# Optimization experiments

Hardware: AMD Instinct MI355X
Metric: run time of the kernel (lower is better)

Reference implementation:

```python
import jax, jax.numpy as jnp
import numpy as np

D_MODEL, D_STATE, N_HEADS = 1024, 64, 16


def setup_inputs() -> dict:
    key = jax.random.key(0)
    ks = jax.random.split(key, 4)
    B, T = 4, 4096
    s = 1.0 / np.sqrt(D_MODEL)
    x = jax.random.normal(ks[0], (B, T, D_MODEL), dtype=jnp.float32)
    h_prev = jnp.zeros((B, N_HEADS, D_STATE), dtype=jnp.float32)
    gate_w = jax.random.normal(ks[1], (2 * N_HEADS * D_STATE, D_MODEL), dtype=jnp.float32) * s
    # torch init: forget-gate bias = 1, input-gate bias = 0
    gate_b = jnp.concatenate([jnp.ones(N_HEADS * D_STATE), jnp.zeros(N_HEADS * D_STATE)]).astype(jnp.float32)
    value_w = jax.random.normal(ks[2], (N_HEADS * D_STATE, D_MODEL), dtype=jnp.float32) * s
    out_w = jax.random.normal(ks[3], (D_MODEL, N_HEADS * D_STATE), dtype=jnp.float32) * s
    return {"x": x, "h_prev": h_prev, "gate_w": gate_w, "gate_b": gate_b, "value_w": value_w, "out_w": out_w}


def reference(x, h_prev, gate_w, gate_b, value_w, out_w):
    B, T, _ = x.shape
    H, S = N_HEADS, D_STATE
    gates = (jnp.einsum('btd,gd->btg', x, gate_w) + gate_b).reshape(B, T, 2, H, S)
    A = jax.nn.sigmoid(gates[:, :, 0])   # [B,T,H,S] forget gate
    Bg = jax.nn.sigmoid(gates[:, :, 1])  # [B,T,H,S] input gate
    V = jnp.einsum('btd,vd->btv', x, value_w).reshape(B, T, H, S)

    def step(h, inp):
        a_t, bv_t = inp
        h = a_t * h + bv_t
        return h, h

    # time-major for scan; precompute B*V elementwise product
    a_tm = jnp.moveaxis(A, 1, 0)                # [T,B,H,S]
    bv_tm = jnp.moveaxis(Bg * V, 1, 0)          # [T,B,H,S]
    h_last, h_seq = jax.lax.scan(step, h_prev, (a_tm, bv_tm))
    h_flat = jnp.moveaxis(h_seq, 0, 1).reshape(B, T, H * S)
    y = jnp.einsum('btv,dv->btd', h_flat, out_w)  # dropout is identity at p=0/eval
    return y, h_last
```

## Files before the change

### kernel.cpp

```cpp
#include <hip/hip_runtime.h>
#include <cstdint>
#include <cstddef>


typedef __bf16 bf16;
typedef __bf16 bf16x8 __attribute__((ext_vector_type(8)));
typedef float  f32x4  __attribute__((ext_vector_type(4)));

__device__ __forceinline__ void gload_lds16(const void* g, void* l) {
  __builtin_amdgcn_global_load_lds(
      (const __attribute__((address_space(1))) void*)g,
      (__attribute__((address_space(3))) void*)l, 16, 0, 0);
}

__device__ __forceinline__ float sigmoidf_(float x) {
  return 1.0f / (1.0f + __expf(-x));
}

__global__ __launch_bounds__(256) void cast_f32_to_bf16(
    const float* __restrict__ src, bf16* __restrict__ dst, int n8) {
  int i = blockIdx.x * 256 + threadIdx.x;
  if (i >= n8) return;
  const float4* s4 = (const float4*)src;
  float4 v0 = s4[2 * i], v1 = s4[2 * i + 1];
  bf16x8 o;
  o[0] = (bf16)v0.x; o[1] = (bf16)v0.y; o[2] = (bf16)v0.z; o[3] = (bf16)v0.w;
  o[4] = (bf16)v1.x; o[5] = (bf16)v1.y; o[6] = (bf16)v1.z; o[7] = (bf16)v1.w;
  *(bf16x8*)(dst + (size_t)i * 8) = o;
}

template <int MCOLS, int EPI>
__global__ __launch_bounds__(256, 3) void gemm_bt(
    const bf16* __restrict__ A, const bf16* __restrict__ Bw,
    const float* __restrict__ gate_b,
    float* __restrict__ o0, float* __restrict__ o1, float* __restrict__ o2) {
  constexpr int K = 1024;
  __shared__ __align__(16) bf16 As[128 * 64];
  __shared__ __align__(16) bf16 Bs[128 * 64];
  const int tid  = threadIdx.x;
  const int lane = tid & 63;
  const int quad = lane >> 4;
  const int wv   = tid >> 6;
  const int wrow = wv & 1, wcol = wv >> 1;
  const int n0 = blockIdx.y * 128;
  const int m0 = blockIdx.x * 128;

  const bf16* ga[4];
  const bf16* gb[4];
  bf16* la[4];
  bf16* lb[4];
#pragma unroll
  for (int j = 0; j < 4; ++j) {
    int s   = j * 256 + tid;
    int row = s >> 3;
    int kc  = (s & 7) ^ (row & 7);
    ga[j] = A  + (size_t)(n0 + row) * K + kc * 8;
    gb[j] = Bw + (size_t)(m0 + row) * K + kc * 8;
    la[j] = &As[s * 8];
    lb[j] = &Bs[s * 8];
  }

  f32x4 acc[4][4];
#pragma unroll
  for (int mi = 0; mi < 4; ++mi)
#pragma unroll
    for (int ni = 0; ni < 4; ++ni) acc[mi][ni] = (f32x4){0.f, 0.f, 0.f, 0.f};

  for (int k0 = 0; k0 < K; k0 += 64) {
#pragma unroll
    for (int j = 0; j < 4; ++j) gload_lds16(ga[j], la[j]);
#pragma unroll
    for (int j = 0; j < 4; ++j) gload_lds16(gb[j], lb[j]);
#pragma unroll
    for (int j = 0; j < 4; ++j) { ga[j] += 64; gb[j] += 64; }
    __syncthreads();
#pragma unroll
    for (int kk = 0; kk < 2; ++kk) {
      bf16x8 af[4], bfv[4];
#pragma unroll
      for (int mi = 0; mi < 4; ++mi) {
        int row  = wrow * 64 + mi * 16 + (lane & 15);
        int slot = row * 8 + ((kk * 4 + quad) ^ (row & 7));
        af[mi] = *(const bf16x8*)(&As[slot * 8]);
      }
#pragma unroll
      for (int ni = 0; ni < 4; ++ni) {
        int row  = wcol * 64 + ni * 16 + (lane & 15);
        int slot = row * 8 + ((kk * 4 + quad) ^ (row & 7));
        bfv[ni] = *(const bf16x8*)(&Bs[slot * 8]);
      }
#pragma unroll
      for (int mi = 0; mi < 4; ++mi)
#pragma unroll
        for (int ni = 0; ni < 4; ++ni)
          acc[mi][ni] = __builtin_amdgcn_mfma_f32_16x16x32_bf16(
              af[mi], bfv[ni], acc[mi][ni], 0, 0, 0);
    }
    __syncthreads();
  }

#pragma unroll
  for (int mi = 0; mi < 4; ++mi) {
#pragma unroll
    for (int ni = 0; ni < 4; ++ni) {
      const int m = m0 + wcol * 64 + ni * 16 + (lane & 15);
#pragma unroll
      for (int r = 0; r < 4; ++r) {
        const int n = n0 + wrow * 64 + mi * 16 + quad * 4 + r;
        float val = acc[mi][ni][r];
        if (EPI == 0) {
          if (m < 2048) {
            float sv = sigmoidf_(val + gate_b[m]);
            if (m < 1024)
              o0[(size_t)n * 1024 + m] = sv;
            else
              o1[(size_t)n * 1024 + (m - 1024)] = sv;
          } else {
            o2[(size_t)n * 1024 + (m - 2048)] = val;
          }
        } else {
          o0[(size_t)n * MCOLS + m] = val;
        }
      }
    }
  }
}

__global__ __launch_bounds__(256) void scan_pass1(
    const float* __restrict__ a, const float* __restrict__ bg,
    const float* __restrict__ v, float* __restrict__ Ac,
    float* __restrict__ Uc) {
  const int c = blockIdx.x * 256 + threadIdx.x;
  const int j = blockIdx.y;
  const int b = blockIdx.z;
  const size_t base = ((size_t)(b * 4096 + j * 128)) * 1024 + c;
  const float* pa = a + base;
  const float* pg = bg + base;
  const float* pv = v + base;
  float P = 1.f, U = 0.f;
#pragma unroll 4
  for (int t = 0; t < 128; ++t) {
    float at  = pa[(size_t)t * 1024];
    float bvt = pg[(size_t)t * 1024] * pv[(size_t)t * 1024];
    P *= at;
    U = at * U + bvt;
  }
  const size_t o = ((size_t)(b * 32 + j)) * 1024 + c;
  Ac[o] = P;
  Uc[o] = U;
}

__global__ __launch_bounds__(256) void scan_pass2(
    const float* __restrict__ Ac, const float* __restrict__ Uc,
    const float* __restrict__ h_prev, float* __restrict__ Hs,
    float* __restrict__ hlast) {
  const int id = blockIdx.x * 256 + threadIdx.x;
  const int b = id >> 10, c = id & 1023;
  float H = h_prev[b * 1024 + c];
  for (int j = 0; j < 32; ++j) {
    const size_t o = ((size_t)(b * 32 + j)) * 1024 + c;
    Hs[o] = H;
    H = Ac[o] * H + Uc[o];
  }
  hlast[b * 1024 + c] = H;
}

__global__ __launch_bounds__(256) void scan_pass3(
    const float* __restrict__ a, const float* __restrict__ bg,
    const float* __restrict__ v, const float* __restrict__ Hs,
    bf16* __restrict__ hb) {
  const int c = blockIdx.x * 256 + threadIdx.x;
  const int j = blockIdx.y;
  const int b = blockIdx.z;
  const size_t base = ((size_t)(b * 4096 + j * 128)) * 1024 + c;
  const float* pa = a + base;
  const float* pg = bg + base;
  const float* pv = v + base;
  bf16* ph = hb + base;
  float h = Hs[((size_t)(b * 32 + j)) * 1024 + c];
#pragma unroll 4
  for (int t = 0; t < 128; ++t) {
    float at  = pa[(size_t)t * 1024];
    float bvt = pg[(size_t)t * 1024] * pv[(size_t)t * 1024];
    h = at * h + bvt;
    ph[(size_t)t * 1024] = (bf16)h;
  }
}

extern "C" void kernel_launch(void* const* d_in, const int* in_sizes, int n_in,
                              void* d_out, int out_size, void* d_ws,
                              size_t ws_size, hipStream_t stream) {
  const float* x       = (const float*)d_in[0];
  const float* h_prev  = (const float*)d_in[1];
  const float* gate_w  = (const float*)d_in[2];
  const float* gate_b  = (const float*)d_in[3];
  const float* value_w = (const float*)d_in[4];
  const float* out_w   = (const float*)d_in[5];
  float* out = (float*)d_out;

  char* ws = (char*)d_ws;
  bf16*  xb   = (bf16*)(ws);
  bf16*  wgv  = (bf16*)(ws + 33554432);
  bf16*  owb  = (bf16*)(ws + 39845888);
  float* g1   = (float*)(ws + 41943040);
  float* vbuf = (float*)(ws + 109051904);
  float* Ac   = (float*)(ws + 176160768);
  float* Uc   = (float*)(ws + 176685056);
  float* Hs   = (float*)(ws + 177209344);
  bf16*  hb   = xb;
  float* abuf = out;
  float* hlast = out + 16777216;

  cast_f32_to_bf16<<<8192, 256, 0, stream>>>(x, xb, 2097152);
  cast_f32_to_bf16<<<1024, 256, 0, stream>>>(gate_w, wgv, 262144);
  cast_f32_to_bf16<<<512, 256, 0, stream>>>(value_w, wgv + 2048 * 1024, 131072);
  cast_f32_to_bf16<<<512, 256, 0, stream>>>(out_w, owb, 131072);

  gemm_bt<3072, 0><<<dim3(24, 128), 256, 0, stream>>>(xb, wgv, gate_b, abuf,
                                                      g1, vbuf);

  scan_pass1<<<dim3(4, 32, 4), 256, 0, stream>>>(abuf, g1, vbuf, Ac, Uc);
  scan_pass2<<<16, 256, 0, stream>>>(Ac, Uc, h_prev, Hs, hlast);
  scan_pass3<<<dim3(4, 32, 4), 256, 0, stream>>>(abuf, g1, vbuf, Hs, hb);

  gemm_bt<1024, 1><<<dim3(8, 128), 256, 0, stream>>>(hb, owb, nullptr, out,
                                                     nullptr, nullptr);
}
```

Measured before the change: 406.2 us.

## Store gate and value intermediates in fp16 and switch GEMMs to f16 MFMA

Switches the GEMM operands from bf16 to fp16 and writes the sigmoid gates and value projections as fp16 instead of fp32, halving intermediate traffic between the gate GEMM and the scan passes. The scan passes now read f16x2 pairs, with each thread handling two channels, and accumulate in fp32. This trades reduced memory bandwidth for lower-precision storage of the gates and values, and fp16 range limits could affect accuracy.

```diff
diff --git a/kernel.cpp b/kernel.cpp
--- a/kernel.cpp
+++ b/kernel.cpp
@@ -3,9 +3,10 @@
 #include <cstddef>
 
 
-typedef __bf16 bf16;
-typedef __bf16 bf16x8 __attribute__((ext_vector_type(8)));
-typedef float  f32x4  __attribute__((ext_vector_type(4)));
+typedef _Float16 f16;
+typedef _Float16 f16x2 __attribute__((ext_vector_type(2)));
+typedef _Float16 f16x8 __attribute__((ext_vector_type(8)));
+typedef float    f32x4 __attribute__((ext_vector_type(4)));
 
 __device__ __forceinline__ void gload_lds16(const void* g, void* l) {
   __builtin_amdgcn_global_load_lds(
@@ -17,26 +18,26 @@
   return 1.0f / (1.0f + __expf(-x));
 }
 
-__global__ __launch_bounds__(256) void cast_f32_to_bf16(
-    const float* __restrict__ src, bf16* __restrict__ dst, int n8) {
+__global__ __launch_bounds__(256) void cast_f32_to_f16(
+    const float* __restrict__ src, f16* __restrict__ dst, int n8) {
   int i = blockIdx.x * 256 + threadIdx.x;
   if (i >= n8) return;
   const float4* s4 = (const float4*)src;
   float4 v0 = s4[2 * i], v1 = s4[2 * i + 1];
-  bf16x8 o;
-  o[0] = (bf16)v0.x; o[1] = (bf16)v0.y; o[2] = (bf16)v0.z; o[3] = (bf16)v0.w;
-  o[4] = (bf16)v1.x; o[5] = (bf16)v1.y; o[6] = (bf16)v1.z; o[7] = (bf16)v1.w;
-  *(bf16x8*)(dst + (size_t)i * 8) = o;
-}
-
-template <int MCOLS, int EPI>
+  f16x8 o;
+  o[0] = (f16)v0.x; o[1] = (f16)v0.y; o[2] = (f16)v0.z; o[3] = (f16)v0.w;
+  o[4] = (f16)v1.x; o[5] = (f16)v1.y; o[6] = (f16)v1.z; o[7] = (f16)v1.w;
+  *(f16x8*)(dst + (size_t)i * 8) = o;
+}
+
+template <int EPI>
 __global__ __launch_bounds__(256, 3) void gemm_bt(
-    const bf16* __restrict__ A, const bf16* __restrict__ Bw,
+    const f16* __restrict__ A, const f16* __restrict__ Bw,
     const float* __restrict__ gate_b,
-    float* __restrict__ o0, float* __restrict__ o1, float* __restrict__ o2) {
+    void* __restrict__ o0v, void* __restrict__ o1v, void* __restrict__ o2v) {
   constexpr int K = 1024;
-  __shared__ __align__(16) bf16 As[128 * 64];
-  __shared__ __align__(16) bf16 Bs[128 * 64];
+  __shared__ __align__(16) f16 As[128 * 64];
+  __shared__ __align__(16) f16 Bs[128 * 64];
   const int tid  = threadIdx.x;
   const int lane = tid & 63;
   const int quad = lane >> 4;
@@ -45,10 +46,10 @@
   const int n0 = blockIdx.y * 128;
   const int m0 = blockIdx.x * 128;
 
-  const bf16* ga[4];
-  const bf16* gb[4];
-  bf16* la[4];
-  bf16* lb[4];
+  const f16* ga[4];
+  const f16* gb[4];
+  f16* la[4];
+  f16* lb[4];
 #pragma unroll
   for (int j = 0; j < 4; ++j) {
     int s   = j * 256 + tid;
@@ -76,24 +77,24 @@
     __syncthreads();
 #pragma unroll
     for (int kk = 0; kk < 2; ++kk) {
-      bf16x8 af[4], bfv[4];
+      f16x8 af[4], bfv[4];
 #pragma unroll
       for (int mi = 0; mi < 4; ++mi) {
         int row  = wrow * 64 + mi * 16 + (lane & 15);
         int slot = row * 8 + ((kk * 4 + quad) ^ (row & 7));
-        af[mi] = *(const bf16x8*)(&As[slot * 8]);
+        af[mi] = *(const f16x8*)(&As[slot * 8]);
       }
 #pragma unroll
       for (int ni = 0; ni < 4; ++ni) {
         int row  = wcol * 64 + ni * 16 + (lane & 15);
         int slot = row * 8 + ((kk * 4 + quad) ^ (row & 7));
-        bfv[ni] = *(const bf16x8*)(&Bs[slot * 8]);
+        bfv[ni] = *(const f16x8*)(&Bs[slot * 8]);
       }
 #pragma unroll
       for (int mi = 0; mi < 4; ++mi)
 #pragma unroll
         for (int ni = 0; ni < 4; ++ni)
-          acc[mi][ni] = __builtin_amdgcn_mfma_f32_16x16x32_bf16(
+          acc[mi][ni] = __builtin_amdgcn_mfma_f32_16x16x32_f16(
               af[mi], bfv[ni], acc[mi][ni], 0, 0, 0);
     }
     __syncthreads();
@@ -110,16 +111,16 @@
         float val = acc[mi][ni][r];
         if (EPI == 0) {
           if (m < 2048) {
-            float sv = sigmoidf_(val + gate_b[m]);
+            f16 sv = (f16)sigmoidf_(val + gate_b[m]);
             if (m < 1024)
-              o0[(size_t)n * 1024 + m] = sv;
+              ((f16*)o0v)[(size_t)n * 1024 + m] = sv;
             else
-              o1[(size_t)n * 1024 + (m - 1024)] = sv;
+              ((f16*)o1v)[(size_t)n * 1024 + (m - 1024)] = sv;
           } else {
-            o2[(size_t)n * 1024 + (m - 2048)] = val;
+            ((f16*)o2v)[(size_t)n * 1024 + (m - 2048)] = (f16)val;
           }
         } else {
-          o0[(size_t)n * MCOLS + m] = val;
+          ((float*)o0v)[(size_t)n * 1024 + m] = val;
         }
       }
     }
@@ -127,27 +128,28 @@
 }
 
 __global__ __launch_bounds__(256) void scan_pass1(
-    const float* __restrict__ a, const float* __restrict__ bg,
-    const float* __restrict__ v, float* __restrict__ Ac,
-    float* __restrict__ Uc) {
-  const int c = blockIdx.x * 256 + threadIdx.x;
+    const f16x2* __restrict__ a, const f16x2* __restrict__ bg,
+    const f16x2* __restrict__ v, float2* __restrict__ Ac,
+    float2* __restrict__ Uc) {
+  const int c2 = blockIdx.x * 256 + threadIdx.x;
   const int j = blockIdx.y;
   const int b = blockIdx.z;
-  const size_t base = ((size_t)(b * 4096 + j * 128)) * 1024 + c;
-  const float* pa = a + base;
-  const float* pg = bg + base;
-  const float* pv = v + base;
-  float P = 1.f, U = 0.f;
+  const size_t base = ((size_t)(b * 4096 + j * 128)) * 512 + c2;
+  float P0 = 1.f, P1 = 1.f, U0 = 0.f, U1 = 0.f;
 #pragma unroll 4
   for (int t = 0; t < 128; ++t) {
-    float at  = pa[(size_t)t * 1024];
-    float bvt = pg[(size_t)t * 1024] * pv[(size_t)t * 1024];
-    P *= at;
-    U = at * U + bvt;
-  }
-  const size_t o = ((size_t)(b * 32 + j)) * 1024 + c;
-  Ac[o] = P;
-  Uc[o] = U;
+    const size_t o = base + (size_t)t * 512;
+    f16x2 at = a[o], gt = bg[o], vt = v[o];
+    float a0 = (float)at[0], a1 = (float)at[1];
+    float bv0 = (float)gt[0] * (float)vt[0];
+    float bv1 = (float)gt[1] * (float)vt[1];
+    P0 *= a0; P1 *= a1;
+    U0 = a0 * U0 + bv0;
+    U1 = a1 * U1 + bv1;
+  }
+  const size_t o = ((size_t)(b * 32 + j)) * 512 + c2;
+  Ac[o] = make_float2(P0, P1);
+  Uc[o] = make_float2(U0, U1);
 }
 
 __global__ __launch_bounds__(256) void scan_pass2(
@@ -166,24 +168,24 @@
 }
 
 __global__ __launch_bounds__(256) void scan_pass3(
-    const float* __restrict__ a, const float* __restrict__ bg,
-    const float* __restrict__ v, const float* __restrict__ Hs,
-    bf16* __restrict__ hb) {
-  const int c = blockIdx.x * 256 + threadIdx.x;
+    const f16x2* __restrict__ a, const f16x2* __restrict__ bg,
+    const f16x2* __restrict__ v, const float2* __restrict__ Hs,
+    f16x2* __restrict__ hb) {
+  const int c2 = blockIdx.x * 256 + threadIdx.x;
   const int j = blockIdx.y;
   const int b = blockIdx.z;
-  const size_t base = ((size_t)(b * 4096 + j * 128)) * 1024 + c;
-  const float* pa = a + base;
-  const float* pg = bg + base;
-  const float* pv = v + base;
-  bf16* ph = hb + base;
-  float h = Hs[((size_t)(b * 32 + j)) * 1024 + c];
+  const size_t base = ((size_t)(b * 4096 + j * 128)) * 512 + c2;
+  float2 H = Hs[((size_t)(b * 32 + j)) * 512 + c2];
+  float h0 = H.x, h1 = H.y;
 #pragma unroll 4
   for (int t = 0; t < 128; ++t) {
-    float at  = pa[(size_t)t * 1024];
-    float bvt = pg[(size_t)t * 1024] * pv[(size_t)t * 1024];
-    h = at * h + bvt;
-    ph[(size_t)t * 1024] = (bf16)h;
+    const size_t o = base + (size_t)t * 512;
+    f16x2 at = a[o], gt = bg[o], vt = v[o];
+    float a0 = (float)at[0], a1 = (float)at[1];
+    h0 = a0 * h0 + (float)gt[0] * (float)vt[0];
+    h1 = a1 * h1 + (float)gt[1] * (float)vt[1];
+    f16x2 hv; hv[0] = (f16)h0; hv[1] = (f16)h1;
+    hb[o] = hv;
   }
 }
 
@@ -199,30 +201,33 @@
   float* out = (float*)d_out;
 
   char* ws = (char*)d_ws;
-  bf16*  xb   = (bf16*)(ws);
-  bf16*  wgv  = (bf16*)(ws + 33554432);
-  bf16*  owb  = (bf16*)(ws + 39845888);
-  float* g1   = (float*)(ws + 41943040);
-  float* vbuf = (float*)(ws + 109051904);
-  float* Ac   = (float*)(ws + 176160768);
-  float* Uc   = (float*)(ws + 176685056);
-  float* Hs   = (float*)(ws + 177209344);
-  bf16*  hb   = xb;
-  float* abuf = out;
+  f16*   xh   = (f16*)(ws);
+  f16*   wgv  = (f16*)(ws + 33554432);
+  f16*   owb  = (f16*)(ws + 39845888);
+  f16*   abuf = (f16*)(ws + 41943040);
+  f16*   g1   = (f16*)(ws + 75497472);
+  f16*   vbuf = (f16*)(ws + 109051904);
+  float* Ac   = (float*)(ws + 142606336);
+  float* Uc   = (float*)(ws + 143130624);
+  float* Hs   = (float*)(ws + 143654912);
   float* hlast = out + 16777216;
 
-  cast_f32_to_bf16<<<8192, 256, 0, stream>>>(x, xb, 2097152);
-  cast_f32_to_bf16<<<1024, 256, 0, stream>>>(gate_w, wgv, 262144);
-  cast_f32_to_bf16<<<512, 256, 0, stream>>>(value_w, wgv + 2048 * 1024, 131072);
-  cast_f32_to_bf16<<<512, 256, 0, stream>>>(out_w, owb, 131072);
-
-  gemm_bt<3072, 0><<<dim3(24, 128), 256, 0, stream>>>(xb, wgv, gate_b, abuf,
-                                                      g1, vbuf);
-
-  scan_pass1<<<dim3(4, 32, 4), 256, 0, stream>>>(abuf, g1, vbuf, Ac, Uc);
+  cast_f32_to_f16<<<8192, 256, 0, stream>>>(x, xh, 2097152);
+  cast_f32_to_f16<<<1024, 256, 0, stream>>>(gate_w, wgv, 262144);
+  cast_f32_to_f16<<<512, 256, 0, stream>>>(value_w, wgv + 2048 * 1024, 131072);
+  cast_f32_to_f16<<<512, 256, 0, stream>>>(out_w, owb, 131072);
+
+  gemm_bt<0><<<dim3(24, 128), 256, 0, stream>>>(xh, wgv, gate_b, abuf, g1,
+                                                vbuf);
+
+  scan_pass1<<<dim3(2, 32, 4), 256, 0, stream>>>(
+      (const f16x2*)abuf, (const f16x2*)g1, (const f16x2*)vbuf, (float2*)Ac,
+      (float2*)Uc);
   scan_pass2<<<16, 256, 0, stream>>>(Ac, Uc, h_prev, Hs, hlast);
-  scan_pass3<<<dim3(4, 32, 4), 256, 0, stream>>>(abuf, g1, vbuf, Hs, hb);
-
-  gemm_bt<1024, 1><<<dim3(8, 128), 256, 0, stream>>>(hb, owb, nullptr, out,
-                                                     nullptr, nullptr);
-}
+  scan_pass3<<<dim3(2, 32, 4), 256, 0, stream>>>(
+      (const f16x2*)abuf, (const f16x2*)g1, (const f16x2*)vbuf,
+      (const float2*)Hs, (f16x2*)xh);
+
+  gemm_bt<1><<<dim3(8, 128), 256, 0, stream>>>(xh, owb, nullptr, out, nullptr,
+                                               nullptr);
+}
```

After: 377.3 us. -7.1%, faster.
